# Performance work log

Measured on AMD Instinct MI355X. Metric: run time of the kernel, lower is better.

The kernel has to match this reference:

```python
import jax, jax.numpy as jnp
import numpy as np

N_NODES = 100000
N_EDGES = 3200000
D_IN = 128
D_HID = 128


def setup_inputs() -> dict:
    key = jax.random.key(0)
    k1, k2, k3 = jax.random.split(key, 3)
    x = jax.random.normal(k1, (N_NODES, D_IN), dtype=jnp.float32)
    edge_index = jax.random.randint(k2, (2, N_EDGES), 0, N_NODES, dtype=jnp.int64)
    W = jax.random.normal(k3, (D_IN, D_HID), dtype=jnp.float32) * (1.0 / np.sqrt(D_IN))
    b = jnp.zeros((D_HID,), dtype=jnp.float32)
    return {"x": x, "edge_index": edge_index, "W": W, "b": b}


def reference(x, edge_index, W, b):
    N = x.shape[0]
    loop = jnp.arange(N, dtype=edge_index.dtype)
    src = jnp.concatenate([edge_index[0], loop])  # self-loops (PyG default)
    dst = jnp.concatenate([edge_index[1], loop])
    # symmetric normalization D^{-1/2} (A+I) D^{-1/2}
    deg = jax.ops.segment_sum(jnp.ones_like(src, dtype=x.dtype), dst, num_segments=N)
    dinv = jnp.where(deg > 0, jax.lax.rsqrt(deg), 0.0)
    norm = dinv[src] * dinv[dst]  # [E+N]
    h = x @ W  # [N, D_HID] transform before aggregation
    msg = h[src] * norm[:, None]  # gather + scale, [E+N, D_HID]
    agg = jax.ops.segment_sum(msg, dst, num_segments=N)  # scatter-add
    out = jax.nn.relu(agg + b)
    return out  # x_gmm branch is None (gmm not fitted)
```

## Files before the change

kernel.cpp:

```cpp
#include <hip/hip_runtime.h>

#define NN   100000
#define NE   3200000
#define D    128
#define NC   50
#define CSH  11
#define CCAP 67584
#define NF   3200
#define RCAP 1280
#define NSLICE 16
#define P2CAP (CCAP / NSLICE)
#define R1   4096

typedef __attribute__((ext_vector_type(8))) short short8v;
typedef __attribute__((ext_vector_type(4))) float f32x4;

__global__ void k_zero(int* __restrict__ cnt) {
    int i = blockIdx.x * 256 + threadIdx.x;
    if (i < NC + NF) cnt[i] = 0;
}

__global__ __launch_bounds__(256) void k_bin1(const int* __restrict__ src,
                                              const int* __restrict__ dst,
                                              int* __restrict__ gcnt,
                                              unsigned* __restrict__ creg) {
    __shared__ unsigned buf[R1], sorted[R1];
    __shared__ unsigned char bin8[R1], bsort[R1];
    __shared__ int hist[4 * NC], htot[NC], excl[NC], cur[4 * NC], gbase[NC];
    const int t = threadIdx.x, w = t >> 6;
    const int e0 = blockIdx.x * R1;
    const int n = min(R1, NE - e0);

    for (int i = t; i < 4 * NC; i += 256) hist[i] = 0;
    __syncthreads();
    for (int j = t; j < n; j += 256) {
        int d = dst[e0 + j], s = src[e0 + j];
        int b = d >> CSH;
        buf[j] = ((unsigned)(d & 2047) << 17) | (unsigned)s;
        bin8[j] = (unsigned char)b;
        atomicAdd(&hist[w * NC + b], 1);
    }
    __syncthreads();
    if (w == 0) {
        int b = t;
        int h0 = 0, h1 = 0, h2 = 0, h3 = 0, tot = 0;
        if (b < NC) {
            h0 = hist[b]; h1 = hist[NC + b]; h2 = hist[2 * NC + b]; h3 = hist[3 * NC + b];
            tot = h0 + h1 + h2 + h3;
        }
        int sc = tot;
        for (int off = 1; off < 64; off <<= 1) {
            int v = __shfl_up(sc, off, 64);
            if (t >= off) sc += v;
        }
        int ex = sc - tot;
        if (b < NC) {
            excl[b] = ex; htot[b] = tot;
            cur[b] = ex; cur[NC + b] = ex + h0;
            cur[2 * NC + b] = ex + h0 + h1; cur[3 * NC + b] = ex + h0 + h1 + h2;
        }
    }
    __syncthreads();
    for (int j = t; j < n; j += 256) {
        int b = bin8[j];
        int p = atomicAdd(&cur[w * NC + b], 1);
        sorted[p] = buf[j];
        bsort[p] = (unsigned char)b;
    }
    __syncthreads();
    if (t < NC) gbase[t] = htot[t] > 0 ? atomicAdd(&gcnt[t], htot[t]) : 0;
    __syncthreads();
    for (int j = t; j < n; j += 256) {
        int b = bsort[j];
        int p = gbase[b] + (j - excl[b]);
        if (p < CCAP) creg[(size_t)b * CCAP + p] = sorted[j];
    }
}

__global__ __launch_bounds__(256) void k_bin2(const int* __restrict__ gcnt,
                                              const unsigned* __restrict__ creg,
                                              int* __restrict__ fcnt,
                                              unsigned* __restrict__ freg) {
    __shared__ unsigned buf[P2CAP], sorted[P2CAP];
    __shared__ unsigned char bin8[P2CAP], bsort[P2CAP];
    __shared__ int hist[4 * 64], htot[64], excl[64], cur[4 * 64], gbase[64];
    const int t = threadIdx.x, w = t >> 6;
    const int c = blockIdx.x >> 4;
    const int sl = blockIdx.x & (NSLICE - 1);
    const int cnt = min(gcnt[c], CCAP);
    const int slice = (cnt + NSLICE - 1) / NSLICE;
    const int j0 = sl * slice;
    const int n = max(0, min(slice, cnt - j0));
    const unsigned* reg = creg + (size_t)c * CCAP + j0;

    for (int i = t; i < 4 * 64; i += 256) hist[i] = 0;
    __syncthreads();
    for (int j = t; j < n; j += 256) {
        unsigned v = reg[j];
        int b = (v >> 22) & 63;
        buf[j] = v;
        bin8[j] = (unsigned char)b;
        atomicAdd(&hist[w * 64 + b], 1);
    }
    __syncthreads();
    if (w == 0) {
        int b = t;
        int h0 = hist[b], h1 = hist[64 + b], h2 = hist[128 + b], h3 = hist[192 + b];
        int tot = h0 + h1 + h2 + h3;
        int sc = tot;
        for (int off = 1; off < 64; off <<= 1) {
            int v = __shfl_up(sc, off, 64);
            if (t >= off) sc += v;
        }
        int ex = sc - tot;
        excl[b] = ex; htot[b] = tot;
        cur[b] = ex; cur[64 + b] = ex + h0;
        cur[128 + b] = ex + h0 + h1; cur[192 + b] = ex + h0 + h1 + h2;
    }
    __syncthreads();
    for (int j = t; j < n; j += 256) {
        int b = bin8[j];
        int p = atomicAdd(&cur[w * 64 + b], 1);
        sorted[p] = buf[j];
        bsort[p] = (unsigned char)b;
    }
    __syncthreads();
    if (t < 64) gbase[t] = htot[t] > 0 ? atomicAdd(&fcnt[c * 64 + t], htot[t]) : 0;
    __syncthreads();
    for (int j = t; j < n; j += 256) {
        int b = bsort[j];
        int p = gbase[b] + (j - excl[b]);
        if (p < RCAP) freg[(size_t)(c * 64 + b) * RCAP + p] = sorted[j];
    }
}

__global__ __launch_bounds__(256) void k_deg(const int* __restrict__ fcnt,
                                             const unsigned* __restrict__ freg,
                                             float* __restrict__ dinv) {
    __shared__ int hist[32];
    const int f = blockIdx.x, t = threadIdx.x;
    if (f * 32 >= NN) return;
    if (t < 32) hist[t] = 0;
    __syncthreads();
    const int n = min(fcnt[f], RCAP);
    const unsigned* reg = freg + (size_t)f * RCAP;
    for (int j = t; j < n; j += 256)
        atomicAdd(&hist[(reg[j] >> 17) & 31], 1);
    __syncthreads();
    if (t < 32) {
        int node = f * 32 + t;
        if (node < NN) dinv[node] = rsqrtf(1.0f + (float)hist[t]);
    }
}

__device__ __forceinline__ unsigned bf16_rne(float f) {
    unsigned u = __float_as_uint(f);
    u += 0x7fffu + ((u >> 16) & 1u);
    return u >> 16;
}

#define SWZ(row, kb) (((((row) << 8) | ((kb) << 1))) ^ ((((row) & 7)) << 4))

__global__ __launch_bounds__(256) void k_gemm(const float* __restrict__ x,
                                              const float* __restrict__ W,
                                              const float* __restrict__ dinv,
                                              unsigned* __restrict__ h2, int nrows) {
    __shared__ short xs[128 * 128];
    __shared__ short wt[128 * 128];
    const int t = threadIdx.x;
    const int row0 = blockIdx.x * 128;

    {
        const int n = t & 127, kh = (t >> 7) * 64;
        for (int j = 0; j < 8; ++j) {
            int k0 = kh + j * 8;
            short8v pk;
#pragma unroll
            for (int e = 0; e < 8; ++e)
                pk[e] = (short)bf16_rne(W[(k0 + e) * 128 + n]);
            *(short8v*)&wt[SWZ(n, k0) >> 1] = pk;
        }
    }
    for (int p = 0; p < 8; ++p) {
        int idx = p * 256 + t;
        int r = idx >> 4, k8 = (idx & 15) * 8;
        int row = row0 + r;
        short8v pk = {0, 0, 0, 0, 0, 0, 0, 0};
        if (row < nrows) {
            float4 v0 = *(const float4*)&x[(size_t)row * D + k8];
            float4 v1 = *(const float4*)&x[(size_t)row * D + k8 + 4];
            pk[0] = (short)bf16_rne(v0.x); pk[1] = (short)bf16_rne(v0.y);
            pk[2] = (short)bf16_rne(v0.z); pk[3] = (short)bf16_rne(v0.w);
            pk[4] = (short)bf16_rne(v1.x); pk[5] = (short)bf16_rne(v1.y);
            pk[6] = (short)bf16_rne(v1.z); pk[7] = (short)bf16_rne(v1.w);
        }
        *(short8v*)&xs[SWZ(r, k8) >> 1] = pk;
    }
    __syncthreads();

    const int w = t >> 6, l = t & 63;
    const int lr = l & 15, lg = l >> 4;

    f32x4 acc[2][8];
#pragma unroll
    for (int i = 0; i < 2; ++i)
#pragma unroll
        for (int j = 0; j < 8; ++j)
            acc[i][j] = (f32x4){0.f, 0.f, 0.f, 0.f};

#pragma unroll
    for (int ks = 0; ks < 4; ++ks) {
        const int kb = ks * 32 + lg * 8;
        short8v a0 = *(const short8v*)&xs[SWZ(w * 32 + lr, kb) >> 1];
        short8v a1 = *(const short8v*)&xs[SWZ(w * 32 + 16 + lr, kb) >> 1];
#pragma unroll
        for (int nt = 0; nt < 8; ++nt) {
            short8v bv = *(const short8v*)&wt[SWZ(nt * 16 + lr, kb) >> 1];
            acc[0][nt] = __builtin_amdgcn_mfma_f32_16x16x32_bf16(a0, bv, acc[0][nt], 0, 0, 0);
            acc[1][nt] = __builtin_amdgcn_mfma_f32_16x16x32_bf16(a1, bv, acc[1][nt], 0, 0, 0);
        }
    }

#pragma unroll
    for (int rt = 0; rt < 2; ++rt) {
#pragma unroll
        for (int rg = 0; rg < 4; ++rg) {
            int row = row0 + w * 32 + rt * 16 + lg * 4 + rg;
            float di = (row < nrows) ? dinv[row] : 0.f;
#pragma unroll
            for (int nt = 0; nt < 8; ++nt) {
                unsigned u = bf16_rne(acc[rt][nt][rg] * di);
                unsigned o = (unsigned)__shfl_xor((int)u, 1);
                if (!(lr & 1) && row < nrows)
                    h2[(size_t)row * 64 + nt * 8 + (lr >> 1)] = u | (o << 16);
            }
        }
    }
}

__device__ __forceinline__ float lo_f(unsigned v) { return __uint_as_float(v << 16); }
__device__ __forceinline__ float hi_f(unsigned v) { return __uint_as_float(v & 0xffff0000u); }

__global__ __launch_bounds__(256) void k_agg(const unsigned* __restrict__ h2,
                                             const float* __restrict__ dinv,
                                             const int* __restrict__ fcnt,
                                             const unsigned* __restrict__ freg,
                                             const float* __restrict__ bias,
                                             float* __restrict__ out) {
    __shared__ unsigned buf[RCAP], sorted[RCAP];
    __shared__ int hist[256], cur[256], excl[257];
    const int f = blockIdx.x, t = threadIdx.x;
    const int node0 = f * 32;
    if (node0 >= NN) return;
    const int n = min(fcnt[f], RCAP);
    const unsigned* reg = freg + (size_t)f * RCAP;

    hist[t] = 0;
    __syncthreads();
    for (int j = t; j < n; j += 256) {
        unsigned v = reg[j];
        buf[j] = v;
        int key = (int)(((v >> 17) & 31u) * 8u + ((v >> 14) & 7u));
        atomicAdd(&hist[key], 1);
    }
    __syncthreads();
    if (t < 64) {
        int h0 = hist[t * 4], h1 = hist[t * 4 + 1];
        int h2v = hist[t * 4 + 2], h3 = hist[t * 4 + 3];
        int s = h0 + h1 + h2v + h3;
        int sc = s;
        for (int off = 1; off < 64; off <<= 1) {
            int v = __shfl_up(sc, off, 64);
            if (t >= off) sc += v;
        }
        int base = sc - s;
        excl[t * 4] = base;                cur[t * 4] = base;
        excl[t * 4 + 1] = base + h0;       cur[t * 4 + 1] = base + h0;
        excl[t * 4 + 2] = base + h0 + h1;  cur[t * 4 + 2] = base + h0 + h1;
        excl[t * 4 + 3] = base + h0 + h1 + h2v; cur[t * 4 + 3] = base + h0 + h1 + h2v;
        if (t == 63) excl[256] = sc;
    }
    __syncthreads();
    for (int j = t; j < n; j += 256) {
        unsigned v = buf[j];
        int key = (int)(((v >> 17) & 31u) * 8u + ((v >> 14) & 7u));
        int p = atomicAdd(&cur[key], 1);
        sorted[p] = v;
    }
    __syncthreads();

    const int w = t >> 6, lane = t & 63;
    const int g = lane >> 4;
    const int q = lane & 15;

#define ADD8(V) do { \
        acc[0] += lo_f((V).x); acc[1] += hi_f((V).x); \
        acc[2] += lo_f((V).y); acc[3] += hi_f((V).y); \
        acc[4] += lo_f((V).z); acc[5] += hi_f((V).z); \
        acc[6] += lo_f((V).w); acc[7] += hi_f((V).w); } while (0)

    for (int i = 0; i < 8; ++i) {
        const int dl = w * 8 + i;
        const int node = node0 + dl;
        if (node >= NN) break;
        const int start = excl[dl * 8];
        const int end = excl[(dl + 1) * 8];

        float acc[8] = {0.f, 0.f, 0.f, 0.f, 0.f, 0.f, 0.f, 0.f};
        if (g == 0) {
            uint4 v = *(const uint4*)&h2[(size_t)node * 64 + q * 4];
            ADD8(v);
        }
        int base = start;
        for (; base + 8 <= end; base += 8) {
            int s0 = (int)(sorted[base + g]     & 0x1FFFFu);
            int s1 = (int)(sorted[base + 4 + g] & 0x1FFFFu);
            uint4 v0 = *(const uint4*)&h2[(size_t)s0 * 64 + q * 4];
            uint4 v1 = *(const uint4*)&h2[(size_t)s1 * 64 + q * 4];
            ADD8(v0);
            ADD8(v1);
        }
        for (; base < end; base += 4) {
            int e = base + g;
            if (e < end) {
                int s = (int)(sorted[e] & 0x1FFFFu);
                uint4 v = *(const uint4*)&h2[(size_t)s * 64 + q * 4];
                ADD8(v);
            }
        }
#pragma unroll
        for (int k = 0; k < 8; ++k) {
            acc[k] += __shfl_xor(acc[k], 16);
            acc[k] += __shfl_xor(acc[k], 32);
        }
        const float di = dinv[node];
        const int c = q * 8 + g * 2;
        float2 bb = *(const float2*)&bias[c];
        float2 r;
        r.x = fmaxf(di * acc[g * 2]     + bb.x, 0.f);
        r.y = fmaxf(di * acc[g * 2 + 1] + bb.y, 0.f);
        *(float2*)&out[(size_t)node * D + c] = r;
    }
#undef ADD8
}

extern "C" void kernel_launch(void* const* d_in, const int* in_sizes, int n_in,
                              void* d_out, int out_size, void* d_ws, size_t ws_size,
                              hipStream_t stream) {
    const float* x  = (const float*)d_in[0];
    const int*   ei = (const int*)d_in[1];
    const float* W  = (const float*)d_in[2];
    const float* b  = (const float*)d_in[3];
    float* out = (float*)d_out;

    unsigned* h2   = (unsigned*)d_ws;
    float*    dinv = (float*)(h2 + (size_t)NN * 64);
    int*      gcnt = (int*)(dinv + NN);
    int*      fcnt = gcnt + NC;
    unsigned* creg = (unsigned*)(fcnt + NF);
    unsigned* freg = creg + (size_t)NC * CCAP;

    const int* src = ei;
    const int* dst = ei + NE;

    k_zero<<<(NC + NF + 255) / 256, 256, 0, stream>>>(gcnt);
    k_bin1<<<(NE + R1 - 1) / R1, 256, 0, stream>>>(src, dst, gcnt, creg);
    k_bin2<<<NC * NSLICE, 256, 0, stream>>>(gcnt, creg, fcnt, freg);
    k_deg <<<NF, 256, 0, stream>>>(fcnt, freg, dinv);
    k_gemm<<<(NN + 127) / 128, 256, 0, stream>>>(x, W, dinv, h2, NN);
    k_agg <<<NF, 256, 0, stream>>>(h2, dinv, fcnt, freg, b, out);
}
```

Baseline: 199.0 us.

## Use nontemporal loads/stores for streamed buffers and load GEMM A-operand directly to registers

Edge arrays, bin regions and the final output are now read and written with nontemporal hints, so single-use streaming data is kept from polluting cache that the h2 gathers depend on. Separately, the GEMM no longer stages x through shared memory. Each lane loads and converts its own A fragments straight from global memory into registers. This halves LDS use per block and drops one LDS round-trip, at the cost of less coalesced global loads and more registers.

```diff
diff --git a/kernel.cpp b/kernel.cpp
--- a/kernel.cpp
+++ b/kernel.cpp
@@ -14,6 +14,7 @@
 
 typedef __attribute__((ext_vector_type(8))) short short8v;
 typedef __attribute__((ext_vector_type(4))) float f32x4;
+typedef __attribute__((ext_vector_type(2))) float f32x2;
 
 __global__ void k_zero(int* __restrict__ cnt) {
     int i = blockIdx.x * 256 + threadIdx.x;
@@ -34,7 +35,8 @@
     for (int i = t; i < 4 * NC; i += 256) hist[i] = 0;
     __syncthreads();
     for (int j = t; j < n; j += 256) {
-        int d = dst[e0 + j], s = src[e0 + j];
+        int d = __builtin_nontemporal_load(&dst[e0 + j]);
+        int s = __builtin_nontemporal_load(&src[e0 + j]);
         int b = d >> CSH;
         buf[j] = ((unsigned)(d & 2047) << 17) | (unsigned)s;
         bin8[j] = (unsigned char)b;
@@ -73,7 +75,8 @@
     for (int j = t; j < n; j += 256) {
         int b = bsort[j];
         int p = gbase[b] + (j - excl[b]);
-        if (p < CCAP) creg[(size_t)b * CCAP + p] = sorted[j];
+        if (p < CCAP)
+            __builtin_nontemporal_store(sorted[j], &creg[(size_t)b * CCAP + p]);
     }
 }
 
@@ -96,7 +99,7 @@
     for (int i = t; i < 4 * 64; i += 256) hist[i] = 0;
     __syncthreads();
     for (int j = t; j < n; j += 256) {
-        unsigned v = reg[j];
+        unsigned v = __builtin_nontemporal_load(&reg[j]);
         int b = (v >> 22) & 63;
         buf[j] = v;
         bin8[j] = (unsigned char)b;
@@ -130,7 +133,9 @@
     for (int j = t; j < n; j += 256) {
         int b = bsort[j];
         int p = gbase[b] + (j - excl[b]);
-        if (p < RCAP) freg[(size_t)(c * 64 + b) * RCAP + p] = sorted[j];
+        if (p < RCAP)
+            __builtin_nontemporal_store(sorted[j],
+                                        &freg[(size_t)(c * 64 + b) * RCAP + p]);
     }
 }
 
@@ -145,7 +150,7 @@
     const int n = min(fcnt[f], RCAP);
     const unsigned* reg = freg + (size_t)f * RCAP;
     for (int j = t; j < n; j += 256)
-        atomicAdd(&hist[(reg[j] >> 17) & 31], 1);
+        atomicAdd(&hist[(__builtin_nontemporal_load(&reg[j]) >> 17) & 31], 1);
     __syncthreads();
     if (t < 32) {
         int node = f * 32 + t;
@@ -161,11 +166,21 @@
 
 #define SWZ(row, kb) (((((row) << 8) | ((kb) << 1))) ^ ((((row) & 7)) << 4))
 
+__device__ __forceinline__ short8v cvt8(const float* p) {
+    float4 v0 = *(const float4*)p;
+    float4 v1 = *(const float4*)(p + 4);
+    short8v r;
+    r[0] = (short)bf16_rne(v0.x); r[1] = (short)bf16_rne(v0.y);
+    r[2] = (short)bf16_rne(v0.z); r[3] = (short)bf16_rne(v0.w);
+    r[4] = (short)bf16_rne(v1.x); r[5] = (short)bf16_rne(v1.y);
+    r[6] = (short)bf16_rne(v1.z); r[7] = (short)bf16_rne(v1.w);
+    return r;
+}
+
 __global__ __launch_bounds__(256) void k_gemm(const float* __restrict__ x,
                                               const float* __restrict__ W,
                                               const float* __restrict__ dinv,
                                               unsigned* __restrict__ h2, int nrows) {
-    __shared__ short xs[128 * 128];
     __shared__ short wt[128 * 128];
     const int t = threadIdx.x;
     const int row0 = blockIdx.x * 128;
@@ -181,25 +196,21 @@
             *(short8v*)&wt[SWZ(n, k0) >> 1] = pk;
         }
     }
-    for (int p = 0; p < 8; ++p) {
-        int idx = p * 256 + t;
-        int r = idx >> 4, k8 = (idx & 15) * 8;
-        int row = row0 + r;
-        short8v pk = {0, 0, 0, 0, 0, 0, 0, 0};
-        if (row < nrows) {
-            float4 v0 = *(const float4*)&x[(size_t)row * D + k8];
-            float4 v1 = *(const float4*)&x[(size_t)row * D + k8 + 4];
-            pk[0] = (short)bf16_rne(v0.x); pk[1] = (short)bf16_rne(v0.y);
-            pk[2] = (short)bf16_rne(v0.z); pk[3] = (short)bf16_rne(v0.w);
-            pk[4] = (short)bf16_rne(v1.x); pk[5] = (short)bf16_rne(v1.y);
-            pk[6] = (short)bf16_rne(v1.z); pk[7] = (short)bf16_rne(v1.w);
-        }
-        *(short8v*)&xs[SWZ(r, k8) >> 1] = pk;
-    }
     __syncthreads();
 
     const int w = t >> 6, l = t & 63;
     const int lr = l & 15, lg = l >> 4;
+    const int r0 = row0 + w * 32 + lr;
+    const int r1 = r0 + 16;
+
+    const short8v z8 = {0, 0, 0, 0, 0, 0, 0, 0};
+    short8v a[2][4];
+#pragma unroll
+    for (int ks = 0; ks < 4; ++ks) {
+        const int kb = ks * 32 + lg * 8;
+        a[0][ks] = (r0 < nrows) ? cvt8(&x[(size_t)r0 * D + kb]) : z8;
+        a[1][ks] = (r1 < nrows) ? cvt8(&x[(size_t)r1 * D + kb]) : z8;
+    }
 
     f32x4 acc[2][8];
 #pragma unroll
@@ -211,13 +222,11 @@
 #pragma unroll
     for (int ks = 0; ks < 4; ++ks) {
         const int kb = ks * 32 + lg * 8;
-        short8v a0 = *(const short8v*)&xs[SWZ(w * 32 + lr, kb) >> 1];
-        short8v a1 = *(const short8v*)&xs[SWZ(w * 32 + 16 + lr, kb) >> 1];
 #pragma unroll
         for (int nt = 0; nt < 8; ++nt) {
             short8v bv = *(const short8v*)&wt[SWZ(nt * 16 + lr, kb) >> 1];
-            acc[0][nt] = __builtin_amdgcn_mfma_f32_16x16x32_bf16(a0, bv, acc[0][nt], 0, 0, 0);
-            acc[1][nt] = __builtin_amdgcn_mfma_f32_16x16x32_bf16(a1, bv, acc[1][nt], 0, 0, 0);
+            acc[0][nt] = __builtin_amdgcn_mfma_f32_16x16x32_bf16(a[0][ks], bv, acc[0][nt], 0, 0, 0);
+            acc[1][nt] = __builtin_amdgcn_mfma_f32_16x16x32_bf16(a[1][ks], bv, acc[1][nt], 0, 0, 0);
         }
     }
 
@@ -258,7 +267,7 @@
     hist[t] = 0;
     __syncthreads();
     for (int j = t; j < n; j += 256) {
-        unsigned v = reg[j];
+        unsigned v = __builtin_nontemporal_load(&reg[j]);
         buf[j] = v;
         int key = (int)(((v >> 17) & 31u) * 8u + ((v >> 14) & 7u));
         atomicAdd(&hist[key], 1);
@@ -336,10 +345,10 @@
         const float di = dinv[node];
         const int c = q * 8 + g * 2;
         float2 bb = *(const float2*)&bias[c];
-        float2 r;
+        f32x2 r;
         r.x = fmaxf(di * acc[g * 2]     + bb.x, 0.f);
         r.y = fmaxf(di * acc[g * 2 + 1] + bb.y, 0.f);
-        *(float2*)&out[(size_t)node * D + c] = r;
+        __builtin_nontemporal_store(r, (f32x2*)&out[(size_t)node * D + c]);
     }
 #undef ADD8
 }
```

New measurement: 213.5 us. 7.3% more time.
